# Kernel optimization log

Hardware: AMD Instinct MI355X
Metric: run time of the kernel (lower is better)

## Reference

```python
import jax, jax.numpy as jnp
import numpy as np

B, S, E, P, L, V, C = 8, 4096, 512, 64, 4, 32000, 2
H = E // 2


def setup_inputs() -> dict:
    key = jax.random.key(0)
    ks = jax.random.split(key, 16)
    std = 0.02
    d = {
        'x': jax.random.randint(ks[0], (B, S), 0, V),
        'emb': jax.random.normal(ks[1], (V, E), jnp.float32) * std,
        'pos': jax.random.normal(ks[2], (S, E), jnp.float32) * std,
        'Wq': jax.random.normal(ks[3], (L, E, P), jnp.float32) * std,
        'Wk': jax.random.normal(ks[4], (L, E, P), jnp.float32) * std,
        'Wv': jax.random.normal(ks[5], (L, E, E), jnp.float32) * std,
        'Wo': jax.random.normal(ks[6], (L, E, E), jnp.float32) * std,
        'ln_g': jnp.ones((L, E), jnp.float32),
        'ln_b': jnp.zeros((L, E), jnp.float32),
        'W1': jax.random.normal(ks[7], (L, E, 4 * E), jnp.float32) * std,
        'b1': jnp.zeros((L, 4 * E), jnp.float32),
        'W2': jax.random.normal(ks[8], (L, 4 * E, E), jnp.float32) * std,
        'b2': jnp.zeros((L, E), jnp.float32),
        'Wh1': jax.random.normal(ks[9], (E, H), jnp.float32) * std,
        'bh1': jnp.zeros((H,), jnp.float32),
        'Wh2': jax.random.normal(ks[10], (H, C), jnp.float32) * std,
        'bh2': jnp.zeros((C,), jnp.float32),
    }
    return d


def _layer_norm(x, g, b, eps=1e-5):
    mu = jnp.mean(x, axis=-1, keepdims=True)
    var = jnp.var(x, axis=-1, keepdims=True)
    return (x - mu) * jax.lax.rsqrt(var + eps) * g + b


def _linear_attention(h, Wq, Wk, Wv, Wo, eps=1e-6):
    # Performer-style non-causal linear attention with elu+1 feature map.
    q = jnp.einsum('bse,ep->bsp', h, Wq)            # [B,S,P]
    k = jnp.einsum('bse,ep->bsp', h, Wk)            # [B,S,P]
    v = jnp.einsum('bse,ef->bsf', h, Wv)            # [B,S,E]
    phi_q = jax.nn.elu(q) + 1.0
    phi_k = jax.nn.elu(k) + 1.0
    kv = jnp.einsum('bsp,bsf->bpf', phi_k, v)        # [B,P,E] linear-time state
    z = jnp.sum(phi_k, axis=1)                       # [B,P]
    num = jnp.einsum('bsp,bpf->bsf', phi_q, kv)      # [B,S,E]
    den = jnp.einsum('bsp,bp->bs', phi_q, z) + eps   # [B,S]
    attn = num / den[..., None]
    return jnp.einsum('bsf,fe->bse', attn, Wo)


def reference(x, emb, pos, Wq, Wk, Wv, Wo, ln_g, ln_b, W1, b1, W2, b2, Wh1, bh1, Wh2, bh2):
    h = emb[x] + pos[None, :x.shape[1], :]
    for l in range(L):
        residual = h
        a = _linear_attention(h, Wq[l], Wk[l], Wv[l], Wo[l])
        n = _layer_norm(a, ln_g[l], ln_b[l])
        m = jax.nn.gelu(jnp.einsum('bse,ef->bsf', n, W1[l]) + b1[l])
        h = jnp.einsum('bsf,fe->bse', m, W2[l]) + b2[l]
        h = h + residual
    pooled = h[:, 0, :]
    y = jax.nn.relu(pooled @ Wh1 + bh1)
    return y @ Wh2 + bh2
```

## Files before the change

kernel.cpp:

```cpp
#include <hip/hip_runtime.h>
#include <stdint.h>

#define BB 8
#define SS 4096
#define EE 512
#define PP 64
#define LL 4
#define FF 2048
#define HH 256
#define BS (BB*SS)
#define NKV 8

typedef unsigned short u16;
typedef __attribute__((ext_vector_type(8))) __bf16 bf16x8;
typedef __attribute__((ext_vector_type(4))) float f32x4;

__device__ __forceinline__ float b2f(u16 u) {
  union { float f; uint32_t u; } v; v.u = ((uint32_t)u) << 16; return v.f;
}
__device__ __forceinline__ u16 f2b(float f) {
  union { float f; uint32_t u; } v; v.f = f;
  uint32_t u = v.u;
  return (u16)((u + 0x7fffu + ((u >> 16) & 1u)) >> 16);
}
__device__ __forceinline__ float gelu_f(float x) {
  const float c = 0.7978845608028654f;
  float t = tanhf(c * (x + 0.044715f * x * x * x));
  return 0.5f * x * (1.0f + t);
}
__device__ __forceinline__ void gload16(const void* g, void* l) {
  auto gp = (const __attribute__((address_space(1))) uint32_t*)(uintptr_t)g;
  auto lp = (__attribute__((address_space(3))) uint32_t*)(uintptr_t)l;
  __builtin_amdgcn_global_load_lds(gp, lp, 16, 0, 0);
}

__global__ __launch_bounds__(256) void zero_kernel(float* __restrict__ p, int n) {
  int i = blockIdx.x * 256 + threadIdx.x;
  if (i < n) p[i] = 0.f;
}

__global__ __launch_bounds__(128) void embed_kernel(const int* __restrict__ x,
                                                    const float* __restrict__ emb,
                                                    const float* __restrict__ pos,
                                                    float* __restrict__ hf,
                                                    u16* __restrict__ hb) {
  int tok = blockIdx.x;
  int t = threadIdx.x;
  int s = tok & (SS - 1);
  int id = x[tok];
  int e = t * 4;
  float4 v = *(const float4*)(emb + (long)id * EE + e);
  float4 p = *(const float4*)(pos + (long)s * EE + e);
  v.x += p.x; v.y += p.y; v.z += p.z; v.w += p.w;
  *(float4*)(hf + (long)tok * EE + e) = v;
  ushort4 u;
  u.x = f2b(v.x); u.y = f2b(v.y); u.z = f2b(v.z); u.w = f2b(v.w);
  *(ushort4*)(hb + (long)tok * EE + e) = u;
}

__global__ __launch_bounds__(256) void transpose_kernel(const float* __restrict__ src,
                                                        u16* __restrict__ dst,
                                                        int R, int C,
                                                        long srcLS, long dstLS, int colOff) {
  __shared__ float tile[32][33];
  int l = blockIdx.z;
  src += (long)l * srcLS;
  dst += (long)l * dstLS;
  int c0 = blockIdx.x * 32, r0 = blockIdx.y * 32;
  int tx = threadIdx.x & 31, ty = threadIdx.x >> 5;
#pragma unroll
  for (int i = 0; i < 32; i += 8)
    tile[ty + i][tx] = src[(long)(r0 + ty + i) * C + c0 + tx];
  __syncthreads();
#pragma unroll
  for (int i = 0; i < 32; i += 8)
    dst[(long)(colOff + c0 + ty + i) * R + r0 + tx] = f2b(tile[tx][ty + i]);
}

struct GemmP {
  const u16* A; const u16* B;
  int M, N, K, lda, ldb, ldc, rowOff;
  long sAz, sBz, sCz;
  float* Cf; u16* Cb;
  const float* bias;
  const float* den; const float* G;
  const float* kwo; const float* vwo;
  float* hf;
};

template<int EPI>
__global__ __launch_bounds__(256) void gemm_nt(GemmP p) {
  __shared__ u16 As[128 * 64];
  __shared__ u16 Bs[128 * 64];
  const int z = blockIdx.z;
  const u16* Ap = p.A + (long)z * p.sAz;
  const u16* Bp = p.B + (long)z * p.sBz;
  const int m0 = blockIdx.y * 128, n0 = blockIdx.x * 128;
  const int t = threadIdx.x;
  const int l = t & 63, w = t >> 6;
  const int wr = w >> 1, wc = w & 1;
  const int r16 = l & 15, kg = l >> 4;
  const int srow = l >> 3;
  const int scw = ((l & 7) ^ srow) * 8;

  f32x4 acc[4][4] = {};

  for (int k0 = 0; k0 < p.K; k0 += 64) {
#pragma unroll
    for (int i = 0; i < 4; ++i) {
      int g = w * 4 + i;
      int row = g * 8 + srow;
      gload16(Ap + (long)(m0 + row) * p.lda + k0 + scw, &As[g * 512]);
      gload16(Bp + (long)(n0 + row) * p.ldb + k0 + scw, &Bs[g * 512]);
    }
    __syncthreads();
#pragma unroll
    for (int ks = 0; ks < 2; ++ks) {
      bf16x8 af[4], bfr[4];
#pragma unroll
      for (int mi = 0; mi < 4; ++mi) {
        int row = wr * 64 + mi * 16 + r16;
        int ch = (ks * 4 + kg) ^ (row & 7);
        af[mi] = *(const bf16x8*)(&As[row * 64 + ch * 8]);
      }
#pragma unroll
      for (int ni = 0; ni < 4; ++ni) {
        int row = wc * 64 + ni * 16 + r16;
        int ch = (ks * 4 + kg) ^ (row & 7);
        bfr[ni] = *(const bf16x8*)(&Bs[row * 64 + ch * 8]);
      }
#pragma unroll
      for (int mi = 0; mi < 4; ++mi)
#pragma unroll
        for (int ni = 0; ni < 4; ++ni)
          acc[mi][ni] = __builtin_amdgcn_mfma_f32_16x16x32_bf16(af[mi], bfr[ni], acc[mi][ni], 0, 0, 0);
    }
    __syncthreads();
  }

#pragma unroll
  for (int mi = 0; mi < 4; ++mi) {
#pragma unroll
    for (int ni = 0; ni < 4; ++ni) {
#pragma unroll
      for (int j = 0; j < 4; ++j) {
        int row = m0 + wr * 64 + mi * 16 + kg * 4 + j;
        int col = n0 + wc * 64 + ni * 16 + r16;
        float v = acc[mi][ni][j];
        long idx = (long)row * p.ldc + col;
        if constexpr (EPI == 0) {
          (p.Cb + (long)z * p.sCz)[idx] = f2b(v > 0.f ? v : expf(v) - 1.f);
        } else if constexpr (EPI == 1) {
          (p.Cb + (long)z * p.sCz)[idx] = f2b(v);
        } else if constexpr (EPI == 2) {
          long grow = p.rowOff + row;
          int b = (int)(grow >> 12);
          float a = (p.kwo[(long)b * EE + col] + p.G[grow] * p.vwo[(long)b * EE + col] + v) / p.den[grow];
          p.Cf[idx] = a;
        } else if constexpr (EPI == 4) {
          p.Cb[idx] = f2b(gelu_f(v + p.bias[col]));
        } else {
          float r = v + p.bias[col] + p.hf[idx];
          p.hf[idx] = r;
          p.Cb[idx] = f2b(r);
        }
      }
    }
  }
}

__global__ __launch_bounds__(256) void kv_mfma(const u16* __restrict__ phi,
                                               const u16* __restrict__ v,
                                               float* __restrict__ kvpart) {
  __shared__ u16 phT[64 * 72];
  __shared__ u16 vTs[128 * 72];
  const int f0 = blockIdx.x * 128;
  const int kidx = blockIdx.y;
  const int b = blockIdx.z;
  const int t = threadIdx.x;
  const int l = t & 63, w = t >> 6;
  const int r16 = l & 15, kg = l >> 4;

  f32x4 acc[4][2] = {};

  for (int kc = 0; kc < (SS / NKV) / 64; ++kc) {
    const long srow = (long)b * SS + kidx * (SS / NKV) + kc * 64;
#pragma unroll
    for (int pass = 0; pass < 2; ++pass) {
      int pp = t & 63;
      int sb = ((t >> 6) << 3) + pass * 32;
      u16 tmp[8];
#pragma unroll
      for (int j = 0; j < 8; ++j)
        tmp[j] = phi[(srow + sb + j) * 128 + 64 + pp];
      uint4 pk;
      pk.x = (uint32_t)tmp[0] | ((uint32_t)tmp[1] << 16);
      pk.y = (uint32_t)tmp[2] | ((uint32_t)tmp[3] << 16);
      pk.z = (uint32_t)tmp[4] | ((uint32_t)tmp[5] << 16);
      pk.w = (uint32_t)tmp[6] | ((uint32_t)tmp[7] << 16);
      *(uint4*)(&phT[pp * 72 + sb]) = pk;
    }
#pragma unroll
    for (int pass = 0; pass < 4; ++pass) {
      int ff = t & 127;
      int sb = ((t >> 7) << 3) + pass * 16;
      u16 tmp[8];
#pragma unroll
      for (int j = 0; j < 8; ++j)
        tmp[j] = v[(srow + sb + j) * EE + f0 + ff];
      uint4 pk;
      pk.x = (uint32_t)tmp[0] | ((uint32_t)tmp[1] << 16);
      pk.y = (uint32_t)tmp[2] | ((uint32_t)tmp[3] << 16);
      pk.z = (uint32_t)tmp[4] | ((uint32_t)tmp[5] << 16);
      pk.w = (uint32_t)tmp[6] | ((uint32_t)tmp[7] << 16);
      *(uint4*)(&vTs[ff * 72 + sb]) = pk;
    }
    __syncthreads();
#pragma unroll
    for (int ks = 0; ks < 2; ++ks) {
      int sloc = ks * 32 + kg * 8;
      bf16x8 af[4], bfr[2];
#pragma unroll
      for (int mi = 0; mi < 4; ++mi)
        af[mi] = *(const bf16x8*)(&phT[(mi * 16 + r16) * 72 + sloc]);
#pragma unroll
      for (int ni = 0; ni < 2; ++ni)
        bfr[ni] = *(const bf16x8*)(&vTs[(w * 32 + ni * 16 + r16) * 72 + sloc]);
#pragma unroll
      for (int mi = 0; mi < 4; ++mi)
#pragma unroll
        for (int ni = 0; ni < 2; ++ni)
          acc[mi][ni] = __builtin_amdgcn_mfma_f32_16x16x32_bf16(af[mi], bfr[ni], acc[mi][ni], 0, 0, 0);
    }
    __syncthreads();
  }

  float* outp = kvpart + ((long)kidx * BB + b) * EE * PP;
#pragma unroll
  for (int mi = 0; mi < 4; ++mi) {
#pragma unroll
    for (int ni = 0; ni < 2; ++ni) {
#pragma unroll
      for (int j = 0; j < 4; ++j) {
        int pidx = mi * 16 + kg * 4 + j;
        int fidx = f0 + w * 32 + ni * 16 + r16;
        outp[(long)fidx * PP + pidx] = acc[mi][ni][j];
      }
    }
  }
}

__global__ __launch_bounds__(256) void kvreduce(const float* __restrict__ kvpart,
                                                float* __restrict__ kvf,
                                                u16* __restrict__ kvb) {
  long i = (long)blockIdx.x * 256 + threadIdx.x;
  const long SKV = (long)BB * EE * PP;
  float s = 0.f;
#pragma unroll
  for (int k = 0; k < NKV; ++k) s += kvpart[k * SKV + i];
  kvf[i] = s;
  kvb[i] = f2b(s);
}

__global__ __launch_bounds__(256) void zg_kernel(const u16* __restrict__ phi, float* __restrict__ zg) {
  int p = blockIdx.x, b = blockIdx.y, t = threadIdx.x;
  float a = 0.f;
  for (int s = t; s < SS; s += 256)
    a += b2f(phi[((long)b * SS + s) * 128 + 64 + p]);
  __shared__ float red[256];
  red[t] = a; __syncthreads();
  for (int o = 128; o > 0; o >>= 1) { if (t < o) red[t] += red[t + o]; __syncthreads(); }
  if (t == 0) zg[b * PP + p] = red[0];
}

__global__ __launch_bounds__(256) void hbar_kernel(const float* __restrict__ hf, float* __restrict__ hb) {
  int f = blockIdx.y * 256 + threadIdx.x;
  int b = blockIdx.x;
  long s0 = blockIdx.z * 256;
  const float* p = hf + ((long)b * SS + s0) * EE + f;
  float a = 0.f;
  for (int s = 0; s < 256; ++s) a += p[(long)s * EE];
  atomicAdd(&hb[b * EE + f], a);
}

__global__ __launch_bounds__(256) void smallmm_kernel(const float* __restrict__ in,
                                                      const float* __restrict__ W,
                                                      float* __restrict__ out) {
  int j = blockIdx.x * 256 + threadIdx.x;
  int b = blockIdx.y;
  const float* ib = in + b * EE;
  float s = 0.f;
  for (int f = 0; f < EE; ++f) s += ib[f] * W[(long)f * EE + j];
  out[b * EE + j] = s;
}

__global__ __launch_bounds__(256) void kbar_kernel(const float* __restrict__ kvf,
                                                   const float* __restrict__ vbar,
                                                   float* __restrict__ kb) {
  int i = blockIdx.x * 256 + threadIdx.x;
  const float* wp = kvf + (long)i * PP;
  float s = 0.f;
#pragma unroll
  for (int p = 0; p < PP; ++p) s += wp[p];
  kb[i] = 64.f * vbar[i] + s;
}

__global__ __launch_bounds__(256) void den_kernel(const u16* __restrict__ phi,
                                                  const float* __restrict__ zg,
                                                  float* __restrict__ den,
                                                  float* __restrict__ G) {
  long row = (long)blockIdx.x * 256 + threadIdx.x;
  int b = (int)(row >> 12);
  const u16* pr = phi + row * 128;
  const float* zb = zg + b * PP;
  float Gs = 0.f, dot = 0.f, Z = 0.f;
#pragma unroll
  for (int c = 0; c < 8; ++c) {
    uint4 q = *(const uint4*)(pr + c * 8);
    u16 uu[8] = {(u16)(q.x & 0xffff), (u16)(q.x >> 16), (u16)(q.y & 0xffff), (u16)(q.y >> 16),
                 (u16)(q.z & 0xffff), (u16)(q.z >> 16), (u16)(q.w & 0xffff), (u16)(q.w >> 16)};
#pragma unroll
    for (int i = 0; i < 8; ++i) {
      float gq = b2f(uu[i]);
      float zz = zb[c * 8 + i];
      Gs += gq; dot += gq * zz; Z += zz;
    }
  }
  den[row] = 64.f * 4096.f + 4096.f * Gs + Z + dot + 1e-6f;
  G[row] = Gs;
}

__global__ __launch_bounds__(256) void ln_kernel(const float* __restrict__ a,
                                                 const float* __restrict__ g,
                                                 const float* __restrict__ beta,
                                                 u16* __restrict__ out) {
  int w = threadIdx.x >> 6, l = threadIdx.x & 63;
  long row = (long)blockIdx.x * 4 + w;
  int e = l * 8;
  const float* x = a + row * EE + e;
  float4 v0 = *(const float4*)(x);
  float4 v1 = *(const float4*)(x + 4);
  float vals[8] = {v0.x, v0.y, v0.z, v0.w, v1.x, v1.y, v1.z, v1.w};
  float sum = 0.f, sq = 0.f;
#pragma unroll
  for (int j = 0; j < 8; ++j) { sum += vals[j]; sq += vals[j] * vals[j]; }
#pragma unroll
  for (int o = 1; o < 64; o <<= 1) {
    sum += __shfl_xor(sum, o, 64);
    sq  += __shfl_xor(sq,  o, 64);
  }
  float mu = sum * (1.f / EE);
  float var = sq * (1.f / EE) - mu * mu;
  float rs = rsqrtf(var + 1e-5f);
  u16 ov[8];
#pragma unroll
  for (int j = 0; j < 8; ++j)
    ov[j] = f2b((vals[j] - mu) * rs * g[e + j] + beta[e + j]);
  *(ushort4*)(out + row * EE + e) = *(ushort4*)&ov[0];
  *(ushort4*)(out + row * EE + e + 4) = *(ushort4*)&ov[4];
}

__global__ __launch_bounds__(256) void last_xi(const u16* __restrict__ phi,
                                               const float* __restrict__ kvf,
                                               float* __restrict__ xi) {
  int f = blockIdx.x * 256 + threadIdx.x;
  int b = blockIdx.y;
  long r = (long)b * SS;
  const float* kp = kvf + ((long)b * EE + f) * PP;
  float s = 0.f;
#pragma unroll
  for (int p = 0; p < PP; ++p) s += b2f(phi[r * 128 + p]) * kp[p];
  xi[b * EE + f] = s;
}
__global__ __launch_bounds__(256) void last_av(const float* __restrict__ xi,
                                               const float* __restrict__ Wo,
                                               const float* __restrict__ kwo,
                                               const float* __restrict__ vwo,
                                               const float* __restrict__ G,
                                               const float* __restrict__ den,
                                               float* __restrict__ av) {
  __shared__ float xis[EE];
  int e = blockIdx.x * 256 + threadIdx.x;
  int b = blockIdx.y;
  xis[threadIdx.x] = xi[b * EE + threadIdx.x];
  xis[threadIdx.x + 256] = xi[b * EE + threadIdx.x + 256];
  __syncthreads();
  float s = 0.f;
  for (int f = 0; f < EE; ++f) s += xis[f] * Wo[(long)f * EE + e];
  long r = (long)b * SS;
  av[b * EE + e] = (kwo[b * EE + e] + G[r] * vwo[b * EE + e] + s) / den[r];
}
__global__ __launch_bounds__(256) void last_ln(const float* __restrict__ av,
                                               const float* __restrict__ g,
                                               const float* __restrict__ beta,
                                               float* __restrict__ nn) {
  __shared__ float red[256];
  int b = blockIdx.x, t = threadIdx.x;
  float v0 = av[b * EE + t], v1 = av[b * EE + t + 256];
  red[t] = v0 + v1; __syncthreads();
  for (int o = 128; o > 0; o >>= 1) { if (t < o) red[t] += red[t + o]; __syncthreads(); }
  float mu = red[0] * (1.f / EE);
  __syncthreads();
  red[t] = v0 * v0 + v1 * v1; __syncthreads();
  for (int o = 128; o > 0; o >>= 1) { if (t < o) red[t] += red[t + o]; __syncthreads(); }
  float var = red[0] * (1.f / EE) - mu * mu;
  float rs = rsqrtf(var + 1e-5f);
  nn[b * EE + t] = (v0 - mu) * rs * g[t] + beta[t];
  nn[b * EE + t + 256] = (v1 - mu) * rs * g[t + 256] + beta[t + 256];
}
__global__ __launch_bounds__(256) void last_w1(const float* __restrict__ nn,
                                               const float* __restrict__ W1,
                                               const float* __restrict__ b1,
                                               float* __restrict__ mm) {
  __shared__ float nns[EE];
  int j = blockIdx.x * 256 + threadIdx.x;
  int b = blockIdx.y;
  nns[threadIdx.x] = nn[b * EE + threadIdx.x];
  nns[threadIdx.x + 256] = nn[b * EE + threadIdx.x + 256];
  __syncthreads();
  float s = b1[j];
  for (int e = 0; e < EE; ++e) s += nns[e] * W1[(long)e * FF + j];
  mm[b * FF + j] = gelu_f(s);
}
__global__ __launch_bounds__(256) void last_w2(const float* __restrict__ mm,
                                               const float* __restrict__ W2,
                                               const float* __restrict__ b2,
                                               const float* __restrict__ hf,
                                               float* __restrict__ hfin) {
  __shared__ float mms[FF];
  int e = blockIdx.x * 256 + threadIdx.x;
  int b = blockIdx.y;
#pragma unroll
  for (int i = 0; i < 8; ++i)
    mms[threadIdx.x + i * 256] = mm[b * FF + threadIdx.x + i * 256];
  __syncthreads();
  float s = b2[e];
  for (int j = 0; j < FF; ++j) s += mms[j] * W2[(long)j * EE + e];
  hfin[b * EE + e] = s + hf[(long)b * SS * EE + e];
}

__global__ __launch_bounds__(256) void head_kernel(const float* __restrict__ hfin,
                                                   const float* __restrict__ Wh1,
                                                   const float* __restrict__ bh1,
                                                   const float* __restrict__ Wh2,
                                                   const float* __restrict__ bh2,
                                                   float* __restrict__ out) {
  int t = threadIdx.x;
  __shared__ float red[256];
  for (int b = 0; b < BB; ++b) {
    const float* pb = hfin + (long)b * EE;
    float a = bh1[t];
    for (int e = 0; e < EE; ++e) a += pb[e] * Wh1[(long)e * HH + t];
    a = fmaxf(a, 0.f);
    for (int c = 0; c < 2; ++c) {
      red[t] = a * Wh2[t * 2 + c];
      __syncthreads();
      for (int o = 128; o > 0; o >>= 1) { if (t < o) red[t] += red[t + o]; __syncthreads(); }
      if (t == 0) out[b * 2 + c] = red[0] + bh2[c];
      __syncthreads();
    }
  }
}

extern "C" void kernel_launch(void* const* d_in, const int* in_sizes, int n_in,
                              void* d_out, int out_size, void* d_ws, size_t ws_size,
                              hipStream_t stream) {
  (void)in_sizes; (void)n_in; (void)out_size;
  const int*   x   = (const int*)d_in[0];
  const float* emb = (const float*)d_in[1];
  const float* pos = (const float*)d_in[2];
  const float* Wq  = (const float*)d_in[3];
  const float* Wk  = (const float*)d_in[4];
  const float* Wv  = (const float*)d_in[5];
  const float* Wo  = (const float*)d_in[6];
  const float* lng = (const float*)d_in[7];
  const float* lnb = (const float*)d_in[8];
  const float* W1  = (const float*)d_in[9];
  const float* b1  = (const float*)d_in[10];
  const float* W2  = (const float*)d_in[11];
  const float* b2  = (const float*)d_in[12];
  const float* Wh1 = (const float*)d_in[13];
  const float* bh1 = (const float*)d_in[14];
  const float* Wh2 = (const float*)d_in[15];
  const float* bh2 = (const float*)d_in[16];
  float* out = (float*)d_out;

  char* ws = (char*)d_ws;
  size_t off = 0;
  auto alloc = [&](size_t bytes) {
    char* p = ws + off;
    off = (off + bytes + 255) & ~(size_t)255;
    return p;
  };
  float* hf   = (float*)alloc((size_t)BS * EE * 4);
  u16*   hb   = (u16*)  alloc((size_t)BS * EE * 2);
  u16*   phi  = (u16*)  alloc((size_t)BS * 128 * 2);
  u16*   sbuf = (u16*)  alloc((size_t)BS * EE * 2);
  float* den  = (float*)alloc((size_t)BS * 4);
  float* Gbuf = (float*)alloc((size_t)BS * 4);
  float* kvpart = (float*)alloc((size_t)NKV * BB * EE * PP * 4);
  float* kvf  = (float*)alloc((size_t)BB * EE * PP * 4 + (size_t)BB * EE * 4);
  float* hbar = kvf + (size_t)BB * EE * PP;
  u16*   kvb  = (u16*)  alloc((size_t)BB * EE * PP * 2);
  float* zg   = (float*)alloc((size_t)BB * PP * 4);
  float* vbar = (float*)alloc((size_t)BB * EE * 4);
  float* kbar = (float*)alloc((size_t)BB * EE * 4);
  float* kwo  = (float*)alloc((size_t)BB * EE * 4);
  float* vwo  = (float*)alloc((size_t)BB * EE * 4);
  float* hfin = (float*)alloc((size_t)BB * EE * 4);
  float* xib  = (float*)alloc((size_t)BB * EE * 4);
  float* avb  = (float*)alloc((size_t)BB * EE * 4);
  float* nnb  = (float*)alloc((size_t)BB * EE * 4);
  float* mmb  = (float*)alloc((size_t)BB * FF * 4);
  u16* wqkT = (u16*)alloc((size_t)LL * 128 * EE * 2);
  u16* wvT  = (u16*)alloc((size_t)LL * EE * EE * 2);
  u16* woT  = (u16*)alloc((size_t)LL * EE * EE * 2);
  u16* w1T  = (u16*)alloc((size_t)LL * FF * EE * 2);
  u16* w2T  = (u16*)alloc((size_t)LL * EE * FF * 2);

  size_t rem = (ws_size > off) ? ws_size - off : 0;
  int CH;
  if ((size_t)BS * FF * 2 <= rem) CH = 1;
  else if (((size_t)BS * EE * 4 + (size_t)BS * FF * 2) / 2 <= rem) CH = 2;
  else if (((size_t)BS * EE * 4 + (size_t)BS * FF * 2) / 4 <= rem) CH = 4;
  else if (((size_t)BS * EE * 4 + (size_t)BS * FF * 2) / 8 <= rem) CH = 8;
  else CH = 16;
  const int MC = BS / CH;
  char* regp = ws + off;
  float* af = (float*)regp;
  u16* mbf = (CH == 1) ? (u16*)regp : (u16*)(regp + (size_t)MC * EE * 4);

  embed_kernel<<<BS, 128, 0, stream>>>(x, emb, pos, hf, hb);
  transpose_kernel<<<dim3(PP/32, EE/32, LL), 256, 0, stream>>>(Wq, wqkT, EE, PP, (long)EE*PP, (long)128*EE, 0);
  transpose_kernel<<<dim3(PP/32, EE/32, LL), 256, 0, stream>>>(Wk, wqkT, EE, PP, (long)EE*PP, (long)128*EE, 64);
  transpose_kernel<<<dim3(EE/32, EE/32, LL), 256, 0, stream>>>(Wv, wvT, EE, EE, (long)EE*EE, (long)EE*EE, 0);
  transpose_kernel<<<dim3(EE/32, EE/32, LL), 256, 0, stream>>>(Wo, woT, EE, EE, (long)EE*EE, (long)EE*EE, 0);
  transpose_kernel<<<dim3(FF/32, EE/32, LL), 256, 0, stream>>>(W1, w1T, EE, FF, (long)EE*FF, (long)FF*EE, 0);
  transpose_kernel<<<dim3(EE/32, FF/32, LL), 256, 0, stream>>>(W2, w2T, FF, EE, (long)FF*EE, (long)EE*FF, 0);

  for (int l = 0; l < LL; ++l) {
    zero_kernel<<<(BB*EE + 255)/256, 256, 0, stream>>>(hbar, BB*EE);
    hbar_kernel<<<dim3(BB, EE/256, 16), 256, 0, stream>>>(hf, hbar);
    smallmm_kernel<<<dim3(EE/256, BB), 256, 0, stream>>>(hbar, Wv + (size_t)l*EE*EE, vbar);
    {
      GemmP p{};
      p.A = hb; p.B = wqkT + (size_t)l * 128 * EE;
      p.M = BS; p.N = 128; p.K = EE;
      p.lda = EE; p.ldb = EE; p.ldc = 128; p.Cb = phi;
      gemm_nt<0><<<dim3(1, BS/128, 1), 256, 0, stream>>>(p);
    }
    {
      GemmP p{};
      p.A = hb; p.B = wvT + (size_t)l * EE * EE;
      p.M = BS; p.N = EE; p.K = EE;
      p.lda = EE; p.ldb = EE; p.ldc = EE; p.Cb = sbuf;
      gemm_nt<1><<<dim3(EE/128, BS/128, 1), 256, 0, stream>>>(p);
    }
    zg_kernel<<<dim3(PP, BB), 256, 0, stream>>>(phi, zg);
    kv_mfma<<<dim3(EE/128, NKV, BB), 256, 0, stream>>>(phi, sbuf, kvpart);
    kvreduce<<<BB*EE*PP/256, 256, 0, stream>>>(kvpart, kvf, kvb);
    kbar_kernel<<<BB*EE/256, 256, 0, stream>>>(kvf, vbar, kbar);
    smallmm_kernel<<<dim3(EE/256, BB), 256, 0, stream>>>(kbar, Wo + (size_t)l*EE*EE, kwo);
    smallmm_kernel<<<dim3(EE/256, BB), 256, 0, stream>>>(vbar, Wo + (size_t)l*EE*EE, vwo);
    den_kernel<<<BS/256, 256, 0, stream>>>(phi, zg, den, Gbuf);
    if (l < LL - 1) {
      {
        GemmP p{};
        p.A = phi; p.B = kvb;
        p.M = SS; p.N = EE; p.K = PP;
        p.lda = 128; p.ldb = PP; p.ldc = EE;
        p.sAz = (long)SS * 128; p.sBz = (long)EE * PP; p.sCz = (long)SS * EE;
        p.Cb = sbuf;
        gemm_nt<1><<<dim3(EE/128, SS/128, BB), 256, 0, stream>>>(p);
      }
      for (int ch = 0; ch < CH; ++ch) {
        int R0 = ch * MC;
        {
          GemmP p{};
          p.A = sbuf + (size_t)R0 * EE; p.B = woT + (size_t)l * EE * EE;
          p.M = MC; p.N = EE; p.K = EE;
          p.lda = EE; p.ldb = EE; p.ldc = EE; p.rowOff = R0;
          p.Cf = af; p.den = den; p.G = Gbuf; p.kwo = kwo; p.vwo = vwo;
          gemm_nt<2><<<dim3(EE/128, MC/128, 1), 256, 0, stream>>>(p);
        }
        ln_kernel<<<MC/4, 256, 0, stream>>>(af, lng + (size_t)l*EE, lnb + (size_t)l*EE, sbuf + (size_t)R0 * EE);
        {
          GemmP p{};
          p.A = sbuf + (size_t)R0 * EE; p.B = w1T + (size_t)l * FF * EE;
          p.M = MC; p.N = FF; p.K = EE;
          p.lda = EE; p.ldb = EE; p.ldc = FF; p.Cb = mbf; p.bias = b1 + (size_t)l * FF;
          gemm_nt<4><<<dim3(FF/128, MC/128, 1), 256, 0, stream>>>(p);
        }
        {
          GemmP p{};
          p.A = mbf; p.B = w2T + (size_t)l * EE * FF;
          p.M = MC; p.N = EE; p.K = FF;
          p.lda = FF; p.ldb = FF; p.ldc = EE;
          p.hf = hf + (size_t)R0 * EE; p.Cb = hb + (size_t)R0 * EE; p.bias = b2 + (size_t)l * EE;
          gemm_nt<5><<<dim3(EE/128, MC/128, 1), 256, 0, stream>>>(p);
        }
      }
    } else {
      last_xi<<<dim3(EE/256, BB), 256, 0, stream>>>(phi, kvf, xib);
      last_av<<<dim3(EE/256, BB), 256, 0, stream>>>(xib, Wo + (size_t)l*EE*EE, kwo, vwo, Gbuf, den, avb);
      last_ln<<<BB, 256, 0, stream>>>(avb, lng + (size_t)l*EE, lnb + (size_t)l*EE, nnb);
      last_w1<<<dim3(FF/256, BB), 256, 0, stream>>>(nnb, W1 + (size_t)l*EE*FF, b1 + (size_t)l*FF, mmb);
      last_w2<<<dim3(EE/256, BB), 256, 0, stream>>>(mmb, W2 + (size_t)l*FF*EE, b2 + (size_t)l*EE, hf, hfin);
    }
  }
  head_kernel<<<1, 256, 0, stream>>>(hfin, Wh1, bh1, Wh2, bh2, out);
}
```

Before: 2.572 ms.

## Write phi and V transposed from GEMM epilogues and split small last-layer matvecs

The phi and V projection GEMMs now also write transposed bf16 copies (phiT, vT) in their epilogues, so the kv reduction kernel can use swizzled 16-byte global-to-LDS loads instead of strided scalar gathers. zg_kernel reads contiguous phiT rows. NKV goes from 8 to 16 to give that kernel more parallelism. The serial last-layer matvecs and the head are split along K into partial-sum kernels plus combine kernels to fill more CUs. In exchange this adds strided 8-byte transposed stores in the epilogues, aliases vT onto the scratch region, and drops the CH=16 option.

New measurement: 2.390 ms. 7.1% less time.

```diff
diff --git a/kernel.cpp b/kernel.cpp
--- a/kernel.cpp
+++ b/kernel.cpp
@@ -9,7 +9,7 @@
 #define FF 2048
 #define HH 256
 #define BS (BB*SS)
-#define NKV 8
+#define NKV 16
 
 typedef unsigned short u16;
 typedef __attribute__((ext_vector_type(8))) __bf16 bf16x8;
@@ -81,7 +81,7 @@
   const u16* A; const u16* B;
   int M, N, K, lda, ldb, ldc, rowOff;
   long sAz, sBz, sCz;
-  float* Cf; u16* Cb;
+  float* Cf; u16* Cb; u16* CbT;
   const float* bias;
   const float* den; const float* G;
   const float* kwo; const float* vwo;
@@ -142,90 +142,103 @@
   for (int mi = 0; mi < 4; ++mi) {
 #pragma unroll
     for (int ni = 0; ni < 4; ++ni) {
-#pragma unroll
-      for (int j = 0; j < 4; ++j) {
-        int row = m0 + wr * 64 + mi * 16 + kg * 4 + j;
-        int col = n0 + wc * 64 + ni * 16 + r16;
-        float v = acc[mi][ni][j];
-        long idx = (long)row * p.ldc + col;
-        if constexpr (EPI == 0) {
-          (p.Cb + (long)z * p.sCz)[idx] = f2b(v > 0.f ? v : expf(v) - 1.f);
-        } else if constexpr (EPI == 1) {
-          (p.Cb + (long)z * p.sCz)[idx] = f2b(v);
-        } else if constexpr (EPI == 2) {
-          long grow = p.rowOff + row;
-          int b = (int)(grow >> 12);
-          float a = (p.kwo[(long)b * EE + col] + p.G[grow] * p.vwo[(long)b * EE + col] + v) / p.den[grow];
-          p.Cf[idx] = a;
-        } else if constexpr (EPI == 4) {
-          p.Cb[idx] = f2b(gelu_f(v + p.bias[col]));
-        } else {
-          float r = v + p.bias[col] + p.hf[idx];
-          p.hf[idx] = r;
-          p.Cb[idx] = f2b(r);
+      const int rowB = m0 + wr * 64 + mi * 16 + kg * 4;
+      const int col  = n0 + wc * 64 + ni * 16 + r16;
+      if constexpr (EPI == 0) {
+        u16 e4[4];
+#pragma unroll
+        for (int j = 0; j < 4; ++j) {
+          float v = acc[mi][ni][j];
+          e4[j] = f2b(v > 0.f ? v : expf(v) - 1.f);
+          p.Cb[(long)(rowB + j) * p.ldc + col] = e4[j];
+        }
+        if (col >= 64) {
+          uint2 pk;
+          pk.x = (uint32_t)e4[0] | ((uint32_t)e4[1] << 16);
+          pk.y = (uint32_t)e4[2] | ((uint32_t)e4[3] << 16);
+          long b = rowB >> 12;
+          *(uint2*)(&p.CbT[((long)(b * 64 + (col - 64))) * SS + (rowB & (SS - 1))]) = pk;
+        }
+      } else if constexpr (EPI == 6) {
+        u16 e4[4];
+#pragma unroll
+        for (int j = 0; j < 4; ++j) e4[j] = f2b(acc[mi][ni][j]);
+        uint2 pk;
+        pk.x = (uint32_t)e4[0] | ((uint32_t)e4[1] << 16);
+        pk.y = (uint32_t)e4[2] | ((uint32_t)e4[3] << 16);
+        long b = rowB >> 12;
+        *(uint2*)(&p.CbT[((long)(b * EE + col)) * SS + (rowB & (SS - 1))]) = pk;
+      } else {
+#pragma unroll
+        for (int j = 0; j < 4; ++j) {
+          int row = rowB + j;
+          float v = acc[mi][ni][j];
+          long idx = (long)row * p.ldc + col;
+          if constexpr (EPI == 1) {
+            (p.Cb + (long)z * p.sCz)[idx] = f2b(v);
+          } else if constexpr (EPI == 2) {
+            long grow = p.rowOff + row;
+            int b = (int)(grow >> 12);
+            float a = (p.kwo[(long)b * EE + col] + p.G[grow] * p.vwo[(long)b * EE + col] + v) / p.den[grow];
+            p.Cf[idx] = a;
+          } else if constexpr (EPI == 4) {
+            p.Cb[idx] = f2b(gelu_f(v + p.bias[col]));
+          } else {
+            float r = v + p.bias[col] + p.hf[idx];
+            p.hf[idx] = r;
+            p.Cb[idx] = f2b(r);
+          }
         }
       }
     }
   }
 }
 
-__global__ __launch_bounds__(256) void kv_mfma(const u16* __restrict__ phi,
-                                               const u16* __restrict__ v,
-                                               float* __restrict__ kvpart) {
-  __shared__ u16 phT[64 * 72];
-  __shared__ u16 vTs[128 * 72];
+__global__ __launch_bounds__(256) void kv_nt(const u16* __restrict__ phiT,
+                                             const u16* __restrict__ vT,
+                                             float* __restrict__ kvpart) {
+  __shared__ u16 As[64 * 64];
+  __shared__ u16 Bs[128 * 64];
   const int f0 = blockIdx.x * 128;
   const int kidx = blockIdx.y;
   const int b = blockIdx.z;
+  const u16* Ap = phiT + (long)b * 64 * SS;
+  const u16* Bp = vT + (long)b * EE * SS;
   const int t = threadIdx.x;
   const int l = t & 63, w = t >> 6;
   const int r16 = l & 15, kg = l >> 4;
+  const int srow = l >> 3;
+  const int scw = ((l & 7) ^ srow) * 8;
 
   f32x4 acc[4][2] = {};
-
-  for (int kc = 0; kc < (SS / NKV) / 64; ++kc) {
-    const long srow = (long)b * SS + kidx * (SS / NKV) + kc * 64;
-#pragma unroll
-    for (int pass = 0; pass < 2; ++pass) {
-      int pp = t & 63;
-      int sb = ((t >> 6) << 3) + pass * 32;
-      u16 tmp[8];
-#pragma unroll
-      for (int j = 0; j < 8; ++j)
-        tmp[j] = phi[(srow + sb + j) * 128 + 64 + pp];
-      uint4 pk;
-      pk.x = (uint32_t)tmp[0] | ((uint32_t)tmp[1] << 16);
-      pk.y = (uint32_t)tmp[2] | ((uint32_t)tmp[3] << 16);
-      pk.z = (uint32_t)tmp[4] | ((uint32_t)tmp[5] << 16);
-      pk.w = (uint32_t)tmp[6] | ((uint32_t)tmp[7] << 16);
-      *(uint4*)(&phT[pp * 72 + sb]) = pk;
-    }
-#pragma unroll
-    for (int pass = 0; pass < 4; ++pass) {
-      int ff = t & 127;
-      int sb = ((t >> 7) << 3) + pass * 16;
-      u16 tmp[8];
-#pragma unroll
-      for (int j = 0; j < 8; ++j)
-        tmp[j] = v[(srow + sb + j) * EE + f0 + ff];
-      uint4 pk;
-      pk.x = (uint32_t)tmp[0] | ((uint32_t)tmp[1] << 16);
-      pk.y = (uint32_t)tmp[2] | ((uint32_t)tmp[3] << 16);
-      pk.z = (uint32_t)tmp[4] | ((uint32_t)tmp[5] << 16);
-      pk.w = (uint32_t)tmp[6] | ((uint32_t)tmp[7] << 16);
-      *(uint4*)(&vTs[ff * 72 + sb]) = pk;
+  const int kbase = kidx * (SS / NKV);
+  for (int k0 = kbase; k0 < kbase + SS / NKV; k0 += 64) {
+#pragma unroll
+    for (int i = 0; i < 2; ++i) {
+      int g = w * 2 + i;
+      gload16(Ap + (long)(g * 8 + srow) * SS + k0 + scw, &As[g * 512]);
+    }
+#pragma unroll
+    for (int i = 0; i < 4; ++i) {
+      int g = w * 4 + i;
+      gload16(Bp + (long)(f0 + g * 8 + srow) * SS + k0 + scw, &Bs[g * 512]);
     }
     __syncthreads();
 #pragma unroll
     for (int ks = 0; ks < 2; ++ks) {
-      int sloc = ks * 32 + kg * 8;
       bf16x8 af[4], bfr[2];
 #pragma unroll
-      for (int mi = 0; mi < 4; ++mi)
-        af[mi] = *(const bf16x8*)(&phT[(mi * 16 + r16) * 72 + sloc]);
-#pragma unroll
-      for (int ni = 0; ni < 2; ++ni)
-        bfr[ni] = *(const bf16x8*)(&vTs[(w * 32 + ni * 16 + r16) * 72 + sloc]);
+      for (int mi = 0; mi < 4; ++mi) {
+        int row = mi * 16 + r16;
+        int ch = (ks * 4 + kg) ^ (row & 7);
+        af[mi] = *(const bf16x8*)(&As[row * 64 + ch * 8]);
+      }
+#pragma unroll
+      for (int ni = 0; ni < 2; ++ni) {
+        int row = w * 32 + ni * 16 + r16;
+        int ch = (ks * 4 + kg) ^ (row & 7);
+        bfr[ni] = *(const bf16x8*)(&Bs[row * 64 + ch * 8]);
+      }
 #pragma unroll
       for (int mi = 0; mi < 4; ++mi)
 #pragma unroll
@@ -237,17 +250,12 @@
 
   float* outp = kvpart + ((long)kidx * BB + b) * EE * PP;
 #pragma unroll
-  for (int mi = 0; mi < 4; ++mi) {
-#pragma unroll
-    for (int ni = 0; ni < 2; ++ni) {
-#pragma unroll
-      for (int j = 0; j < 4; ++j) {
-        int pidx = mi * 16 + kg * 4 + j;
-        int fidx = f0 + w * 32 + ni * 16 + r16;
-        outp[(long)fidx * PP + pidx] = acc[mi][ni][j];
-      }
-    }
-  }
+  for (int mi = 0; mi < 4; ++mi)
+#pragma unroll
+    for (int ni = 0; ni < 2; ++ni)
+#pragma unroll
+      for (int j = 0; j < 4; ++j)
+        outp[(long)(f0 + w * 32 + ni * 16 + r16) * PP + mi * 16 + kg * 4 + j] = acc[mi][ni][j];
 }
 
 __global__ __launch_bounds__(256) void kvreduce(const float* __restrict__ kvpart,
@@ -262,11 +270,19 @@
   kvb[i] = f2b(s);
 }
 
-__global__ __launch_bounds__(256) void zg_kernel(const u16* __restrict__ phi, float* __restrict__ zg) {
+__global__ __launch_bounds__(256) void zg_kernel(const u16* __restrict__ phiT, float* __restrict__ zg) {
   int p = blockIdx.x, b = blockIdx.y, t = threadIdx.x;
+  const u16* row = phiT + ((long)b * 64 + p) * SS + t * 16;
   float a = 0.f;
-  for (int s = t; s < SS; s += 256)
-    a += b2f(phi[((long)b * SS + s) * 128 + 64 + p]);
+#pragma unroll
+  for (int c = 0; c < 2; ++c) {
+    uint4 q = *(const uint4*)(row + c * 8);
+    uint32_t qq[4] = {q.x, q.y, q.z, q.w};
+#pragma unroll
+    for (int i = 0; i < 4; ++i) {
+      a += b2f((u16)(qq[i] & 0xffff)) + b2f((u16)(qq[i] >> 16));
+    }
+  }
   __shared__ float red[256];
   red[t] = a; __syncthreads();
   for (int o = 128; o > 0; o >>= 1) { if (t < o) red[t] += red[t + o]; __syncthreads(); }
@@ -374,29 +390,37 @@
 }
 __global__ __launch_bounds__(256) void last_av(const float* __restrict__ xi,
                                                const float* __restrict__ Wo,
+                                               float* __restrict__ avp) {
+  __shared__ float xis[128];
+  int e = blockIdx.x * 256 + threadIdx.x;
+  int b = blockIdx.y;
+  int f0 = blockIdx.z * 128;
+  if (threadIdx.x < 128) xis[threadIdx.x] = xi[b * EE + f0 + threadIdx.x];
+  __syncthreads();
+  float s = 0.f;
+  for (int f = 0; f < 128; ++f) s += xis[f] * Wo[(long)(f0 + f) * EE + e];
+  avp[((long)blockIdx.z * BB + b) * EE + e] = s;
+}
+__global__ __launch_bounds__(256) void last_ln(const float* __restrict__ avp,
                                                const float* __restrict__ kwo,
                                                const float* __restrict__ vwo,
                                                const float* __restrict__ G,
                                                const float* __restrict__ den,
-                                               float* __restrict__ av) {
-  __shared__ float xis[EE];
-  int e = blockIdx.x * 256 + threadIdx.x;
-  int b = blockIdx.y;
-  xis[threadIdx.x] = xi[b * EE + threadIdx.x];
-  xis[threadIdx.x + 256] = xi[b * EE + threadIdx.x + 256];
-  __syncthreads();
-  float s = 0.f;
-  for (int f = 0; f < EE; ++f) s += xis[f] * Wo[(long)f * EE + e];
-  long r = (long)b * SS;
-  av[b * EE + e] = (kwo[b * EE + e] + G[r] * vwo[b * EE + e] + s) / den[r];
-}
-__global__ __launch_bounds__(256) void last_ln(const float* __restrict__ av,
                                                const float* __restrict__ g,
                                                const float* __restrict__ beta,
                                                float* __restrict__ nn) {
   __shared__ float red[256];
   int b = blockIdx.x, t = threadIdx.x;
-  float v0 = av[b * EE + t], v1 = av[b * EE + t + 256];
+  long r = (long)b * SS;
+  float Gr = G[r], dr = den[r];
+  float v0 = kwo[b * EE + t] + Gr * vwo[b * EE + t];
+  float v1 = kwo[b * EE + t + 256] + Gr * vwo[b * EE + t + 256];
+#pragma unroll
+  for (int c = 0; c < 4; ++c) {
+    v0 += avp[((long)c * BB + b) * EE + t];
+    v1 += avp[((long)c * BB + b) * EE + t + 256];
+  }
+  v0 /= dr; v1 /= dr;
   red[t] = v0 + v1; __syncthreads();
   for (int o = 128; o > 0; o >>= 1) { if (t < o) red[t] += red[t + o]; __syncthreads(); }
   float mu = red[0] * (1.f / EE);
@@ -410,47 +434,74 @@
 }
 __global__ __launch_bounds__(256) void last_w1(const float* __restrict__ nn,
                                                const float* __restrict__ W1,
-                                               const float* __restrict__ b1,
-                                               float* __restrict__ mm) {
-  __shared__ float nns[EE];
+                                               float* __restrict__ mmp) {
+  __shared__ float nns[256];
   int j = blockIdx.x * 256 + threadIdx.x;
   int b = blockIdx.y;
-  nns[threadIdx.x] = nn[b * EE + threadIdx.x];
-  nns[threadIdx.x + 256] = nn[b * EE + threadIdx.x + 256];
+  int e0 = blockIdx.z * 256;
+  nns[threadIdx.x] = nn[b * EE + e0 + threadIdx.x];
   __syncthreads();
-  float s = b1[j];
-  for (int e = 0; e < EE; ++e) s += nns[e] * W1[(long)e * FF + j];
+  float s = 0.f;
+  for (int e = 0; e < 256; ++e) s += nns[e] * W1[(long)(e0 + e) * FF + j];
+  mmp[((long)blockIdx.z * BB + b) * FF + j] = s;
+}
+__global__ __launch_bounds__(256) void last_w1c(const float* __restrict__ mmp,
+                                                const float* __restrict__ b1,
+                                                float* __restrict__ mm) {
+  int j = blockIdx.x * 256 + threadIdx.x;
+  int b = blockIdx.y;
+  float s = b1[j] + mmp[(long)b * FF + j] + mmp[((long)BB + b) * FF + j];
   mm[b * FF + j] = gelu_f(s);
 }
 __global__ __launch_bounds__(256) void last_w2(const float* __restrict__ mm,
                                                const float* __restrict__ W2,
-                                               const float* __restrict__ b2,
-                                               const float* __restrict__ hf,
-                                               float* __restrict__ hfin) {
-  __shared__ float mms[FF];
+                                               float* __restrict__ hfp) {
+  __shared__ float mms[256];
   int e = blockIdx.x * 256 + threadIdx.x;
   int b = blockIdx.y;
-#pragma unroll
-  for (int i = 0; i < 8; ++i)
-    mms[threadIdx.x + i * 256] = mm[b * FF + threadIdx.x + i * 256];
+  int j0 = blockIdx.z * 256;
+  mms[threadIdx.x] = mm[b * FF + j0 + threadIdx.x];
   __syncthreads();
+  float s = 0.f;
+  for (int j = 0; j < 256; ++j) s += mms[j] * W2[(long)(j0 + j) * EE + e];
+  hfp[((long)blockIdx.z * BB + b) * EE + e] = s;
+}
+__global__ __launch_bounds__(256) void last_w2c(const float* __restrict__ hfp,
+                                                const float* __restrict__ b2,
+                                                const float* __restrict__ hf,
+                                                float* __restrict__ hfin) {
+  int e = blockIdx.x * 256 + threadIdx.x;
+  int b = blockIdx.y;
   float s = b2[e];
-  for (int j = 0; j < FF; ++j) s += mms[j] * W2[(long)j * EE + e];
+#pragma unroll
+  for (int jc = 0; jc < 8; ++jc) s += hfp[((long)jc * BB + b) * EE + e];
   hfin[b * EE + e] = s + hf[(long)b * SS * EE + e];
 }
 
-__global__ __launch_bounds__(256) void head_kernel(const float* __restrict__ hfin,
-                                                   const float* __restrict__ Wh1,
-                                                   const float* __restrict__ bh1,
-                                                   const float* __restrict__ Wh2,
-                                                   const float* __restrict__ bh2,
-                                                   float* __restrict__ out) {
+__global__ __launch_bounds__(256) void head1(const float* __restrict__ hfin,
+                                             const float* __restrict__ Wh1,
+                                             float* __restrict__ hp) {
+  __shared__ float hs[128];
+  int j = threadIdx.x;
+  int b = blockIdx.y;
+  int e0 = blockIdx.x * 128;
+  if (j < 128) hs[j] = hfin[b * EE + e0 + j];
+  __syncthreads();
+  float a = 0.f;
+  for (int e = 0; e < 128; ++e) a += hs[e] * Wh1[(long)(e0 + e) * HH + j];
+  hp[((long)blockIdx.x * BB + b) * HH + j] = a;
+}
+__global__ __launch_bounds__(256) void head2(const float* __restrict__ hp,
+                                             const float* __restrict__ bh1,
+                                             const float* __restrict__ Wh2,
+                                             const float* __restrict__ bh2,
+                                             float* __restrict__ out) {
+  __shared__ float red[256];
   int t = threadIdx.x;
-  __shared__ float red[256];
   for (int b = 0; b < BB; ++b) {
-    const float* pb = hfin + (long)b * EE;
     float a = bh1[t];
-    for (int e = 0; e < EE; ++e) a += pb[e] * Wh1[(long)e * HH + t];
+#pragma unroll
+    for (int c = 0; c < 4; ++c) a += hp[((long)c * BB + b) * HH + t];
     a = fmaxf(a, 0.f);
     for (int c = 0; c < 2; ++c) {
       red[t] = a * Wh2[t * 2 + c];
@@ -495,6 +546,7 @@
   float* hf   = (float*)alloc((size_t)BS * EE * 4);
   u16*   hb   = (u16*)  alloc((size_t)BS * EE * 2);
   u16*   phi  = (u16*)  alloc((size_t)BS * 128 * 2);
+  u16*   phiT = (u16*)  alloc((size_t)BB * 64 * SS * 2);
   u16*   sbuf = (u16*)  alloc((size_t)BS * EE * 2);
   float* den  = (float*)alloc((size_t)BS * 4);
   float* Gbuf = (float*)alloc((size_t)BS * 4);
@@ -509,9 +561,12 @@
   float* vwo  = (float*)alloc((size_t)BB * EE * 4);
   float* hfin = (float*)alloc((size_t)BB * EE * 4);
   float* xib  = (float*)alloc((size_t)BB * EE * 4);
-  float* avb  = (float*)alloc((size_t)BB * EE * 4);
   float* nnb  = (float*)alloc((size_t)BB * EE * 4);
+  float* avp  = (float*)alloc((size_t)4 * BB * EE * 4);
+  float* mmp  = (float*)alloc((size_t)2 * BB * FF * 4);
   float* mmb  = (float*)alloc((size_t)BB * FF * 4);
+  float* hfp  = (float*)alloc((size_t)8 * BB * EE * 4);
+  float* hpb  = (float*)alloc((size_t)4 * BB * HH * 4);
   u16* wqkT = (u16*)alloc((size_t)LL * 128 * EE * 2);
   u16* wvT  = (u16*)alloc((size_t)LL * EE * EE * 2);
   u16* woT  = (u16*)alloc((size_t)LL * EE * EE * 2);
@@ -519,14 +574,16 @@
   u16* w2T  = (u16*)alloc((size_t)LL * EE * FF * 2);
 
   size_t rem = (ws_size > off) ? ws_size - off : 0;
+  const size_t vtBytes = (size_t)BB * EE * SS * 2;
   int CH;
   if ((size_t)BS * FF * 2 <= rem) CH = 1;
   else if (((size_t)BS * EE * 4 + (size_t)BS * FF * 2) / 2 <= rem) CH = 2;
   else if (((size_t)BS * EE * 4 + (size_t)BS * FF * 2) / 4 <= rem) CH = 4;
-  else if (((size_t)BS * EE * 4 + (size_t)BS * FF * 2) / 8 <= rem) CH = 8;
-  else CH = 16;
+  else CH = 8;
+  (void)vtBytes;
   const int MC = BS / CH;
   char* regp = ws + off;
+  u16* vT = (u16*)regp;
   float* af = (float*)regp;
   u16* mbf = (CH == 1) ? (u16*)regp : (u16*)(regp + (size_t)MC * EE * 4);
 
@@ -546,18 +603,18 @@
       GemmP p{};
       p.A = hb; p.B = wqkT + (size_t)l * 128 * EE;
       p.M = BS; p.N = 128; p.K = EE;
-      p.lda = EE; p.ldb = EE; p.ldc = 128; p.Cb = phi;
+      p.lda = EE; p.ldb = EE; p.ldc = 128; p.Cb = phi; p.CbT = phiT;
       gemm_nt<0><<<dim3(1, BS/128, 1), 256, 0, stream>>>(p);
     }
     {
       GemmP p{};
       p.A = hb; p.B = wvT + (size_t)l * EE * EE;
       p.M = BS; p.N = EE; p.K = EE;
-      p.lda = EE; p.ldb = EE; p.ldc = EE; p.Cb = sbuf;
-      gemm_nt<1><<<dim3(EE/128, BS/128, 1), 256, 0, stream>>>(p);
-    }
-    zg_kernel<<<dim3(PP, BB), 256, 0, stream>>>(phi, zg);
-    kv_mfma<<<dim3(EE/128, NKV, BB), 256, 0, stream>>>(phi, sbuf, kvpart);
+      p.lda = EE; p.ldb = EE; p.ldc = EE; p.CbT = vT;
+      gemm_nt<6><<<dim3(EE/128, BS/128, 1), 256, 0, stream>>>(p);
+    }
+    zg_kernel<<<dim3(PP, BB), 256, 0, stream>>>(phiT, zg);
+    kv_nt<<<dim3(EE/128, NKV, BB), 256, 0, stream>>>(phiT, vT, kvpart);
     kvreduce<<<BB*EE*PP/256, 256, 0, stream>>>(kvpart, kvf, kvb);
     kbar_kernel<<<BB*EE/256, 256, 0, stream>>>(kvf, vbar, kbar);
     smallmm_kernel<<<dim3(EE/256, BB), 256, 0, stream>>>(kbar, Wo + (size_t)l*EE*EE, kwo);
@@ -602,11 +659,15 @@
       }
     } else {
       last_xi<<<dim3(EE/256, BB), 256, 0, stream>>>(phi, kvf, xib);
-      last_av<<<dim3(EE/256, BB), 256, 0, stream>>>(xib, Wo + (size_t)l*EE*EE, kwo, vwo, Gbuf, den, avb);
-      last_ln<<<BB, 256, 0, stream>>>(avb, lng + (size_t)l*EE, lnb + (size_t)l*EE, nnb);
-      last_w1<<<dim3(FF/256, BB), 256, 0, stream>>>(nnb, W1 + (size_t)l*EE*FF, b1 + (size_t)l*FF, mmb);
-      last_w2<<<dim3(EE/256, BB), 256, 0, stream>>>(mmb, W2 + (size_t)l*FF*EE, b2 + (size_t)l*EE, hf, hfin);
-    }
-  }
-  head_kernel<<<1, 256, 0, stream>>>(hfin, Wh1, bh1, Wh2, bh2, out);
-}
+      last_av<<<dim3(EE/256, BB, 4), 256, 0, stream>>>(xib, Wo + (size_t)l*EE*EE, avp);
+      last_ln<<<BB, 256, 0, stream>>>(avp, kwo, vwo, Gbuf, den,
+                                      lng + (size_t)l*EE, lnb + (size_t)l*EE, nnb);
+      last_w1<<<dim3(FF/256, BB, 2), 256, 0, stream>>>(nnb, W1 + (size_t)l*EE*FF, mmp);
+      last_w1c<<<dim3(FF/256, BB), 256, 0, stream>>>(mmp, b1 + (size_t)l*FF, mmb);
+      last_w2<<<dim3(EE/256, BB, 8), 256, 0, stream>>>(mmb, W2 + (size_t)l*FF*EE, hfp);
+      last_w2c<<<dim3(EE/256, BB), 256, 0, stream>>>(hfp, b2 + (size_t)l*EE, hf, hfin);
+    }
+  }
+  head1<<<dim3(4, BB), 256, 0, stream>>>(hfin, Wh1, hpb);
+  head2<<<1, 256, 0, stream>>>(hpb, bh1, Wh2, bh2, out);
+}
```
